# Performance work log

Hardware: AMD Instinct MI355X
Metric: run time of the kernel (lower is better)

The kernel has to match this reference:

```python
import jax, jax.numpy as jnp
import numpy as np

DIM = 2048
H = 16
DK = DIM // H   # head_k = 128
DV = DIM // H   # head_v = 128
B = 4
N = 4096
INV_SQRT_DK = 1.0 / float(np.sqrt(DK))


def setup_inputs() -> dict:
    key = jax.random.key(0)
    ks = jax.random.split(key, 12)
    s = 0.02
    return {
        "x": jax.random.normal(ks[0], (B, N, DIM), dtype=jnp.float32),
        "M_fast_prev": jax.random.normal(ks[1], (B, H, DK, DV), dtype=jnp.float32) * 0.05,
        "M_slow_prev": jax.random.normal(ks[2], (B, H, DK, DV), dtype=jnp.float32) * 0.05,
        "Wq": jax.random.normal(ks[3], (DIM, H * DK), dtype=jnp.float32) * s,
        "Wk": jax.random.normal(ks[4], (DIM, H * DK), dtype=jnp.float32) * s,
        "Wv": jax.random.normal(ks[5], (DIM, H * DV), dtype=jnp.float32) * s,
        "Wo": jax.random.normal(ks[6], (H * DV, DIM), dtype=jnp.float32) * s,
        "W_bilinear": jax.random.normal(ks[7], (H, DK, DK), dtype=jnp.float32) * 0.02,
        "fast_slope": jnp.full((H, 1, 1), 0.5, dtype=jnp.float32),
        "slow_slope": jnp.full((H, 1, 1), 0.01, dtype=jnp.float32),
        "inter_fast": jnp.full((H, 1, 1), 0.1, dtype=jnp.float32),
        "inter_slow": jnp.full((H, 1, 1), 0.9, dtype=jnp.float32),
        "S_fast": jax.random.normal(ks[8], (H, DK, DK), dtype=jnp.float32) * 0.05,
        "S_slow": jax.random.normal(ks[9], (H, DK, DK), dtype=jnp.float32) * 0.02,
        "f1_w": jax.random.normal(ks[10], (DIM, DIM // 2), dtype=jnp.float32) * s,
        "f1_b": jnp.zeros((DIM // 2,), dtype=jnp.float32),
        "f2_w": jax.random.normal(ks[11], (DIM // 2, H), dtype=jnp.float32) * s,
        "f2_b": jnp.zeros((H,), dtype=jnp.float32),
    }


def reference(x, M_fast_prev, M_slow_prev, Wq, Wk, Wv, Wo, W_bilinear,
              fast_slope, slow_slope, inter_fast, inter_slow,
              S_fast, S_slow, f1_w, f1_b, f2_w, f2_b):
    b, n, _ = x.shape
    # projections -> [b, h, n, d]
    q = (x @ Wq).reshape(b, n, H, DK).transpose(0, 2, 1, 3)
    k = (x @ Wk).reshape(b, n, H, DK).transpose(0, 2, 1, 3)
    v = (x @ Wv).reshape(b, n, H, DV).transpose(0, 2, 1, 3)

    # bilinear resonance modulation of keys
    resonance = jnp.tanh(jnp.einsum('bhnd,hde->bhne', k, W_bilinear))
    k_mod = k * (1.0 + 0.5 * resonance) * INV_SQRT_DK

    # exponential fast/slow decay weights over positions: [h, n, 1]
    idx = (jnp.arange(n, dtype=x.dtype) - (n - 1))[:, None]  # [n, 1]
    fast_w = jnp.exp(fast_slope * idx)  # [h, n, 1]
    slow_w = jnp.exp(slow_slope * idx)

    k_fast = k_mod * fast_w[None]  # [b, h, n, dk]
    k_slow = k_mod * slow_w[None]

    # outer-product state accumulation: [b, h, dk, dv]
    M_fast_curr = jnp.einsum('bhnd,bhnv->bhdv', k_fast, v)
    M_slow_curr = jnp.einsum('bhnd,bhnv->bhdv', k_slow, v)

    # inter-block state carry
    M_fast = M_fast_prev * inter_fast[None] + M_fast_curr
    M_slow = M_slow_prev * inter_slow[None] + M_slow_curr

    # refinement: (I + S) @ M
    eye = jnp.eye(DK, dtype=x.dtype)
    Mf_ref = jnp.einsum('hde,bhev->bhdv', eye[None] + S_fast, M_fast)
    Ms_ref = jnp.einsum('hde,bhev->bhdv', eye[None] + S_slow, M_slow)

    o_fast = jnp.einsum('bhnd,bhdv->bhnv', q, Mf_ref)
    o_slow = jnp.einsum('bhnd,bhdv->bhnv', q, Ms_ref)

    # flux gating from pooled tokens
    h1 = jax.nn.silu(x.mean(axis=1) @ f1_w + f1_b)
    psi = jax.nn.sigmoid(h1 @ f2_w + f2_b)  # [b, h]
    pe = psi[:, :, None, None]

    o_blend = (1.0 - pe) * o_fast + pe * o_slow  # [b, h, n, dv]
    o_blend = o_blend.transpose(0, 2, 1, 3).reshape(b, n, H * DV)
    out = o_blend @ Wo
    return out, M_fast, M_slow, psi
```

## Files before the change

### kernel.cpp

```cpp
#include <hip/hip_runtime.h>
#include <math.h>

typedef __bf16 bf16;
typedef __attribute__((ext_vector_type(8))) __bf16 bf16x8;
typedef __attribute__((ext_vector_type(4))) __bf16 bf16x4;
typedef __attribute__((ext_vector_type(2))) __bf16 bf16x2;
typedef __attribute__((ext_vector_type(4))) float f32x4;

#define DIM 2048
#define NH 16
#define DKK 128
#define BATCH 4
#define SEQ 4096
#define BN (BATCH*SEQ)
#define INV_SQRT_DK 0.08838834764831845f

#define MFMA16(a,b,c) __builtin_amdgcn_mfma_f32_16x16x32_bf16((a),(b),(c),0,0,0)

#define GLDS(gp, lp) __builtin_amdgcn_global_load_lds( \
    (const __attribute__((address_space(1))) void*)(gp), \
    (__attribute__((address_space(3))) void*)(lp), 16, 0, 0)

__device__ inline void stage_tile(const bf16* __restrict__ g, int ld,
                                  bf16* lds, int lane, int wave) {
  const int rl = lane >> 3;
  const int gc = ((lane & 7) ^ (rl & 7)) << 3;
  const bf16* gp = g + (size_t)(wave * 32 + rl) * ld + gc;
#pragma unroll
  for (int t = 0; t < 4; ++t)
    GLDS(gp + (size_t)(t * 8) * ld, lds + (wave * 32 + t * 8) * 64);
}

__device__ inline bf16x8 frag8(const bf16* lds, int r, int kc) {
  return *(const bf16x8*)(lds + r * 64 + (((kc ^ (r & 7)) << 3)));
}

__device__ inline bf16x8 frag8w(const bf16* lds, int r, int kc) {
  return *(const bf16x8*)(lds + r * 128 + (((kc ^ (r & 7)) << 3)));
}
__device__ inline int sqaddr(int r, int c) {
  return r * 128 + ((((c >> 3) ^ (r & 7)) << 3) | (c & 7));
}

__device__ inline float fast_exp(float x) { return __expf(x); }
__device__ inline float fast_tanh(float x) {
  float e2 = __expf(2.f * x);
  return 1.f - 2.f / (e2 + 1.f);
}

__global__ __launch_bounds__(256) void conv_bf16(const float* __restrict__ x,
                                                 bf16* __restrict__ y) {
  int i = (blockIdx.x * 256 + threadIdx.x) * 4;
  float4 v = *(const float4*)(x + i);
  bf16x4 o = { (bf16)v.x, (bf16)v.y, (bf16)v.z, (bf16)v.w };
  *(bf16x4*)(y + i) = o;
}

__global__ __launch_bounds__(256) void tconv3(const float* W0, const float* W1,
                                              const float* W2,
                                              bf16* O0, bf16* O1, bf16* O2) {
  __shared__ float tile[32][33];
  const float* Wp; bf16* Op;
  switch (blockIdx.z) {
    case 0: Wp = W0; Op = O0; break;
    case 1: Wp = W1; Op = O1; break;
    default: Wp = W2; Op = O2; break;
  }
  int c0 = blockIdx.x * 32, r0 = blockIdx.y * 32;
  int tx = threadIdx.x, ty = threadIdx.y;
#pragma unroll
  for (int i = 0; i < 4; ++i)
    tile[ty + i*8][tx] = Wp[(size_t)(r0 + ty + i*8) * DIM + c0 + tx];
  __syncthreads();
#pragma unroll
  for (int i = 0; i < 4; ++i)
    Op[(size_t)(c0 + ty + i*8) * DIM + r0 + tx] = (bf16)tile[tx][ty + i*8];
}

__global__ __launch_bounds__(256) void tconvWb(const float* __restrict__ W,
                                               bf16* __restrict__ Wt) {
  __shared__ float tile[32][33];
  const float* Wp = W + (size_t)blockIdx.z * DKK * DKK;
  bf16* Wtp = Wt + (size_t)blockIdx.z * DKK * DKK;
  int c0 = blockIdx.x * 32, r0 = blockIdx.y * 32;
  int tx = threadIdx.x, ty = threadIdx.y;
#pragma unroll
  for (int i = 0; i < 4; ++i)
    tile[ty + i*8][tx] = Wp[(size_t)(r0 + ty + i*8) * DKK + c0 + tx];
  __syncthreads();
#pragma unroll
  for (int i = 0; i < 4; ++i)
    Wtp[(size_t)(c0 + ty + i*8) * DKK + r0 + tx] = (bf16)tile[tx][ty + i*8];
}

__global__ __launch_bounds__(256) void rweights(const float* __restrict__ fs,
                                                const float* __restrict__ ss,
                                                float* __restrict__ rbuf) {
  int n = blockIdx.x * 256 + threadIdx.x;
  int h = blockIdx.y;
  rbuf[h * SEQ + n] = fast_exp((fs[h] - ss[h]) * (float)(n - (SEQ - 1)));
}

__global__ void zero_f32(float* p, int n) {
  int i = blockIdx.x * 256 + threadIdx.x;
  if (i < n) p[i] = 0.f;
}

__global__ __launch_bounds__(256) void mean_part(const bf16* __restrict__ xb,
                                                 float* __restrict__ xm) {
  int d0 = (blockIdx.x * 256 + threadIdx.x) * 2;
  int b = blockIdx.z;
  const bf16* xp = xb + ((size_t)b * SEQ + (size_t)blockIdx.y * 256) * DIM + d0;
  float s0 = 0.f, s1 = 0.f;
#pragma unroll 8
  for (int n = 0; n < 256; ++n) {
    bf16x2 v = *(const bf16x2*)(xp + (size_t)n * DIM);
    s0 += (float)v[0]; s1 += (float)v[1];
  }
  atomicAdd(&xm[b * DIM + d0], s0);
  atomicAdd(&xm[b * DIM + d0 + 1], s1);
}

__global__ __launch_bounds__(256) void mlp1(const float* __restrict__ xm,
                                            const float* __restrict__ f1w,
                                            float* __restrict__ h1raw) {
  int j = blockIdx.x * 256 + threadIdx.x;
  int b = blockIdx.y;
  int k0 = blockIdx.z * 256;
  const float* xmb = xm + b * DIM + k0;
  const float* w = f1w + (size_t)k0 * (DIM/2) + j;
  float s = 0.f;
#pragma unroll 4
  for (int k = 0; k < 256; ++k) s += xmb[k] * w[(size_t)k * (DIM/2)];
  atomicAdd(&h1raw[b * (DIM/2) + j], s);
}

__global__ void mlp2(const float* __restrict__ h1raw,
                     const float* __restrict__ f1b,
                     const float* __restrict__ f2w,
                     const float* __restrict__ f2b,
                     float* __restrict__ psi_out) {
  int t = threadIdx.x;
  int b = t >> 4, h = t & 15;
  float s = f2b[h];
  for (int k = 0; k < DIM/2; ++k) {
    float hv = h1raw[b * (DIM/2) + k] * (1.f / (float)SEQ) + f1b[k];
    hv = hv / (1.f + fast_exp(-hv));
    s += hv * f2w[k * NH + h];
  }
  psi_out[t] = 1.f / (1.f + fast_exp(-s));
}

template<int MODE>
__global__ __launch_bounds__(256) void gemm_bt(const bf16* __restrict__ A, int lda,
                                               const bf16* __restrict__ Bt, int ldb,
                                               void* __restrict__ Cv, int ldc, int K) {
  __shared__ bf16 sA[128 * 64];
  __shared__ bf16 sB[128 * 64];
  const int tid = threadIdx.x;
  const int lane = tid & 63;
  const int wave = tid >> 6;
  const int quad = lane >> 4;
  const int wm = (wave & 1) * 64;
  const int wn = (wave >> 1) * 64;
  const size_t m0 = (size_t)blockIdx.y * 128;
  const size_t n0 = (size_t)blockIdx.x * 128;
  const bf16* Ap = A;
  const bf16* Bp = Bt;
  size_t mrow = m0;
  size_t cbat = 0;
  if (MODE == 3) Bp += (size_t)(m0 >> 12) * DIM * DIM;
  if (MODE == 4) {
    size_t b = m0 >> 11;
    Ap += b * DIM * DIM;
    cbat = b * DIM * DIM;
    mrow = m0 & 2047;
  }
  f32x4 acc[4][4] = {};
  for (int k0 = 0; k0 < K; k0 += 64) {
    stage_tile(Ap + mrow * lda + k0, lda, sA, lane, wave);
    stage_tile(Bp + n0 * ldb + k0, ldb, sB, lane, wave);
    __syncthreads();
#pragma unroll
    for (int kk = 0; kk < 2; ++kk) {
      const int kc = kk * 4 + quad;
      bf16x8 af[4], bfr[4];
#pragma unroll
      for (int i = 0; i < 4; ++i) af[i] = frag8(sA, wm + i*16 + (lane & 15), kc);
#pragma unroll
      for (int j = 0; j < 4; ++j) bfr[j] = frag8(sB, wn + j*16 + (lane & 15), kc);
#pragma unroll
      for (int i = 0; i < 4; ++i)
#pragma unroll
        for (int j = 0; j < 4; ++j)
          acc[i][j] = MFMA16(af[i], bfr[j], acc[i][j]);
    }
    __syncthreads();
  }
  if (MODE == 2) {
    const int h = (int)(n0 >> 7) & (NH - 1);
    const int b = (int)(m0 >> 12);
    const int nbase0 = (int)(m0 & 4095) + wm + quad * 4;
    bf16* vt = (bf16*)Cv;
#pragma unroll
    for (int i = 0; i < 4; ++i)
#pragma unroll
      for (int j = 0; j < 4; ++j) {
        int dv = wn + j*16 + (lane & 15);
        bf16x4 p = { (bf16)acc[i][j][0], (bf16)acc[i][j][1],
                     (bf16)acc[i][j][2], (bf16)acc[i][j][3] };
        *(bf16x4*)(vt + ((size_t)(b * NH + h) * DKK + dv) * SEQ + nbase0 + i * 16) = p;
      }
  } else {
#pragma unroll
    for (int i = 0; i < 4; ++i)
#pragma unroll
      for (int j = 0; j < 4; ++j) {
        size_t col = n0 + wn + j*16 + (lane & 15);
        size_t row = mrow + wm + i*16 + quad * 4;
#pragma unroll
        for (int r = 0; r < 4; ++r) {
          if (MODE == 3) ((float*)Cv)[(row + r) * ldc + col] = acc[i][j][r];
          else           ((bf16*)Cv)[cbat + (row + r) * ldc + col] = (bf16)acc[i][j][r];
        }
      }
  }
}

__global__ __launch_bounds__(256) void gemm_k_res(const bf16* __restrict__ xb,
                                                  const bf16* __restrict__ Wtk,
                                                  const bf16* __restrict__ Wbt,
                                                  const float* __restrict__ slow_slope,
                                                  bf16* __restrict__ kts) {
  __shared__ bf16 smem[3 * 128 * 64];
  bf16* sA = smem;
  bf16* sB = smem + 8192;
  bf16* K2 = smem;
  bf16* sW = smem + 16384;
  const int tid = threadIdx.x;
  const int lane = tid & 63;
  const int wave = tid >> 6;
  const int quad = lane >> 4;
  const int wm = (wave & 1) * 64;
  const int wn = (wave >> 1) * 64;
  const int h = blockIdx.x;
  const size_t m0 = (size_t)blockIdx.y * 128;
  const int b = (int)(m0 >> 12);
  const int bh = b * NH + h;
  const float ss = slow_slope[h];

  const bf16* Ap = xb + m0 * DIM;
  const bf16* Bp = Wtk + (size_t)h * 128 * DIM;
  f32x4 acc[4][4] = {};
  for (int k0 = 0; k0 < DIM; k0 += 64) {
    stage_tile(Ap + k0, DIM, sA, lane, wave);
    stage_tile(Bp + k0, DIM, sB, lane, wave);
    __syncthreads();
#pragma unroll
    for (int kk = 0; kk < 2; ++kk) {
      const int kc = kk * 4 + quad;
      bf16x8 af[4], bfr[4];
#pragma unroll
      for (int i = 0; i < 4; ++i) af[i] = frag8(sA, wm + i*16 + (lane & 15), kc);
#pragma unroll
      for (int j = 0; j < 4; ++j) bfr[j] = frag8(sB, wn + j*16 + (lane & 15), kc);
#pragma unroll
      for (int i = 0; i < 4; ++i)
#pragma unroll
        for (int j = 0; j < 4; ++j)
          acc[i][j] = MFMA16(af[i], bfr[j], acc[i][j]);
    }
    __syncthreads();
  }
#pragma unroll
  for (int i = 0; i < 4; ++i)
#pragma unroll
    for (int j = 0; j < 4; ++j) {
      int c = wn + j*16 + (lane & 15);
#pragma unroll
      for (int r = 0; r < 4; ++r) {
        int row = wm + i*16 + quad*4 + r;
        K2[sqaddr(row, c)] = (bf16)acc[i][j][r];
      }
    }
  __syncthreads();
  f32x4 accR[4][4] = {};
  const bf16* Wp = Wbt + (size_t)h * DKK * DKK;
#pragma unroll
  for (int k0 = 0; k0 < 128; k0 += 64) {
    stage_tile(Wp + k0, DKK, sW, lane, wave);
    __syncthreads();
#pragma unroll
    for (int kk = 0; kk < 2; ++kk) {
      const int kcl = kk * 4 + quad;
      const int kcg = (k0 >> 3) + kcl;
      bf16x8 af[4], bfr[4];
#pragma unroll
      for (int i = 0; i < 4; ++i) af[i] = frag8w(K2, wm + i*16 + (lane & 15), kcg);
#pragma unroll
      for (int j = 0; j < 4; ++j) bfr[j] = frag8(sW, wn + j*16 + (lane & 15), kcl);
#pragma unroll
      for (int i = 0; i < 4; ++i)
#pragma unroll
        for (int j = 0; j < 4; ++j)
          accR[i][j] = MFMA16(af[i], bfr[j], accR[i][j]);
    }
    __syncthreads();
  }
  float wsv[4][4];
#pragma unroll
  for (int i = 0; i < 4; ++i)
#pragma unroll
    for (int r = 0; r < 4; ++r) {
      int nseq = (int)(m0 & 4095) + wm + i*16 + quad*4 + r;
      wsv[i][r] = fast_exp(ss * (float)(nseq - (SEQ - 1)));
    }
#pragma unroll
  for (int i = 0; i < 4; ++i)
#pragma unroll
    for (int j = 0; j < 4; ++j) {
      int c = wn + j*16 + (lane & 15);
      bf16x4 p;
#pragma unroll
      for (int r = 0; r < 4; ++r) {
        int row = wm + i*16 + quad*4 + r;
        float kv = (float)K2[sqaddr(row, c)];
        float res = fast_tanh(accR[i][j][r]);
        p[r] = (bf16)(kv * (1.f + 0.5f * res) * INV_SQRT_DK * wsv[i][r]);
      }
      int nbase = (int)(m0 & 4095) + wm + i*16 + quad*4;
      *(bf16x4*)(kts + ((size_t)bh * DKK + c) * SEQ + nbase) = p;
    }
}

__global__ __launch_bounds__(256) void mcurr(const bf16* __restrict__ kts,
                                             const bf16* __restrict__ vt,
                                             const float* __restrict__ rbuf,
                                             float* __restrict__ partials) {
  __shared__ bf16 sK[128 * 64];
  __shared__ bf16 sV[128 * 64];
  const int tid = threadIdx.x;
  const int lane = tid & 63;
  const int wave = tid >> 6;
  const int quad = lane >> 4;
  const int wm = (wave & 1) * 64, wn = (wave >> 1) * 64;
  const int s = blockIdx.x;
  const int bh = blockIdx.y;
  const int h = bh & (NH - 1);
  const bf16* Ap = kts + (size_t)bh * DKK * SEQ;
  const bf16* Bp = vt + (size_t)bh * DKK * SEQ;
  const float* rp = rbuf + (size_t)h * SEQ;
  f32x4 accF[4][4] = {}, accS[4][4] = {};
  for (int k0 = s * 512; k0 < s * 512 + 512; k0 += 64) {
    stage_tile(Ap + k0, SEQ, sK, lane, wave);
    stage_tile(Bp + k0, SEQ, sV, lane, wave);
    __syncthreads();
#pragma unroll
    for (int kk = 0; kk < 2; ++kk) {
      const int kc = kk * 4 + quad;
      const int kn = k0 + kc * 8;
      float rv[8];
      *(f32x4*)rv       = *(const f32x4*)(rp + kn);
      *(f32x4*)(rv + 4) = *(const f32x4*)(rp + kn + 4);
      bf16x8 afS[4], afF[4], bfv[4];
#pragma unroll
      for (int i = 0; i < 4; ++i) afS[i] = frag8(sK, wm + i*16 + (lane & 15), kc);
#pragma unroll
      for (int j = 0; j < 4; ++j) bfv[j] = frag8(sV, wn + j*16 + (lane & 15), kc);
#pragma unroll
      for (int i = 0; i < 4; ++i)
#pragma unroll
        for (int e = 0; e < 8; ++e)
          afF[i][e] = (bf16)((float)afS[i][e] * rv[e]);
#pragma unroll
      for (int i = 0; i < 4; ++i)
#pragma unroll
        for (int j = 0; j < 4; ++j) {
          accS[i][j] = MFMA16(afS[i], bfv[j], accS[i][j]);
          accF[i][j] = MFMA16(afF[i], bfv[j], accF[i][j]);
        }
    }
    __syncthreads();
  }
  float* Pf = partials + ((size_t)(s * 64 + bh) * 2 + 0) * (DKK * DKK);
  float* Ps = partials + ((size_t)(s * 64 + bh) * 2 + 1) * (DKK * DKK);
#pragma unroll
  for (int i = 0; i < 4; ++i)
#pragma unroll
    for (int j = 0; j < 4; ++j) {
      int col = wn + j*16 + (lane & 15);
      int row = wm + i*16 + quad * 4;
#pragma unroll
      for (int r = 0; r < 4; ++r) {
        Pf[(row + r) * DKK + col] = accF[i][j][r];
        Ps[(row + r) * DKK + col] = accS[i][j][r];
      }
    }
}

__global__ __launch_bounds__(256) void finalize(const float* __restrict__ partials,
                                                const float* __restrict__ Mf_prev,
                                                const float* __restrict__ Ms_prev,
                                                const float* __restrict__ inter_fast,
                                                const float* __restrict__ inter_slow,
                                                const float* __restrict__ S_fast,
                                                const float* __restrict__ S_slow,
                                                const float* __restrict__ psi,
                                                float* __restrict__ Mf_out,
                                                float* __restrict__ Ms_out,
                                                bf16* __restrict__ Mb) {
  __shared__ float sMf[128 * 33];
  __shared__ float sMs[128 * 33];
  const int t = threadIdx.x;
  const int bh = blockIdx.x;
  const int h = bh & (NH - 1);
  const int e0 = blockIdx.y * 32;
  const int el = t & 31;
  const int d0 = t >> 5;
  const float inf_ = inter_fast[h], ins_ = inter_slow[h];
  const size_t mb = (size_t)bh * (DKK * DKK);
#pragma unroll
  for (int i = 0; i < 16; ++i) {
    int d = d0 + 8 * i;
    int g = d * DKK + e0 + el;
    float mf = inf_ * Mf_prev[mb + g];
    float ms = ins_ * Ms_prev[mb + g];
#pragma unroll
    for (int s = 0; s < 8; ++s) {
      mf += partials[((size_t)(s * 64 + bh) * 2 + 0) * (DKK*DKK) + g];
      ms += partials[((size_t)(s * 64 + bh) * 2 + 1) * (DKK*DKK) + g];
    }
    Mf_out[mb + g] = mf;
    Ms_out[mb + g] = ms;
    sMf[d * 33 + el] = mf;
    sMs[d * 33 + el] = ms;
  }
  __syncthreads();
  const float p = psi[bh];
  for (int i = 0; i < 16; ++i) {
    int d = d0 + 8 * i;
    float accf = sMf[d * 33 + el];
    float accs = sMs[d * 33 + el];
    const float* Sf = S_fast + (size_t)h * (DKK*DKK) + (size_t)d * DKK;
    const float* Ss = S_slow + (size_t)h * (DKK*DKK) + (size_t)d * DKK;
    for (int k = 0; k < DKK; ++k) {
      accf += Sf[k] * sMf[k * 33 + el];
      accs += Ss[k] * sMs[k * 33 + el];
    }
    float blend = (1.f - p) * accf + p * accs;
    Mb[mb + (size_t)d * DKK + e0 + el] = (bf16)blend;
  }
}

__global__ __launch_bounds__(256) void w2_gemm(const bf16* __restrict__ Mb,
                                               const bf16* __restrict__ Wto,
                                               bf16* __restrict__ W2t) {
  __shared__ bf16 sA[128 * 64];
  __shared__ bf16 sB[128 * 64];
  const int tid = threadIdx.x;
  const int lane = tid & 63;
  const int wave = tid >> 6;
  const int quad = lane >> 4;
  const int wm = (wave & 1) * 64, wn = (wave >> 1) * 64;
  const int c0 = blockIdx.x * 128;
  const int bh = blockIdx.y;
  const int h = bh & (NH - 1), b = bh >> 4;
  const bf16* Ap = Mb + (size_t)bh * DKK * DKK;
  const bf16* Bp = Wto + (size_t)c0 * DIM + h * DKK;
  f32x4 acc[4][4] = {};
#pragma unroll
  for (int k0 = 0; k0 < DKK; k0 += 64) {
    stage_tile(Ap + k0, DKK, sA, lane, wave);
    stage_tile(Bp + k0, DIM, sB, lane, wave);
    __syncthreads();
#pragma unroll
    for (int kk = 0; kk < 2; ++kk) {
      const int kc = kk * 4 + quad;
      bf16x8 af[4], bfr[4];
#pragma unroll
      for (int i = 0; i < 4; ++i) af[i] = frag8(sA, wm + i*16 + (lane & 15), kc);
#pragma unroll
      for (int j = 0; j < 4; ++j) bfr[j] = frag8(sB, wn + j*16 + (lane & 15), kc);
#pragma unroll
      for (int i = 0; i < 4; ++i)
#pragma unroll
        for (int j = 0; j < 4; ++j)
          acc[i][j] = MFMA16(af[i], bfr[j], acc[i][j]);
    }
    __syncthreads();
  }
  bf16* base = W2t + (size_t)b * DIM * DIM + h * DKK;
#pragma unroll
  for (int i = 0; i < 4; ++i)
#pragma unroll
    for (int j = 0; j < 4; ++j) {
      int col = wn + j*16 + (lane & 15);
      int row0 = wm + i*16 + quad * 4;
      bf16x4 p = { (bf16)acc[i][j][0], (bf16)acc[i][j][1],
                   (bf16)acc[i][j][2], (bf16)acc[i][j][3] };
      *(bf16x4*)(base + (size_t)(c0 + col) * DIM + row0) = p;
    }
}

extern "C" void kernel_launch(void* const* d_in, const int* in_sizes, int n_in,
                              void* d_out, int out_size, void* d_ws, size_t ws_size,
                              hipStream_t stream) {
  const float* x        = (const float*)d_in[0];
  const float* Mf_prev  = (const float*)d_in[1];
  const float* Ms_prev  = (const float*)d_in[2];
  const float* Wq       = (const float*)d_in[3];
  const float* Wk       = (const float*)d_in[4];
  const float* Wv       = (const float*)d_in[5];
  const float* Wo       = (const float*)d_in[6];
  const float* Wbil     = (const float*)d_in[7];
  const float* fast_slope = (const float*)d_in[8];
  const float* slow_slope = (const float*)d_in[9];
  const float* inter_fast = (const float*)d_in[10];
  const float* inter_slow = (const float*)d_in[11];
  const float* S_fast   = (const float*)d_in[12];
  const float* S_slow   = (const float*)d_in[13];
  const float* f1w      = (const float*)d_in[14];
  const float* f1b      = (const float*)d_in[15];
  const float* f2w      = (const float*)d_in[16];
  const float* f2b      = (const float*)d_in[17];

  char* ws = (char*)d_ws;
  bf16*  xb       = (bf16*)(ws);
  float* partials = (float*)(ws + 67108864);
  bf16*  W2t      = (bf16*)(ws + 67108864);
  bf16*  Wcombt   = (bf16*)(ws + 100663296);
  bf16*  Wqb      = (bf16*)(ws + 134217728);
  bf16*  Wtk      = (bf16*)(ws + 142606336);
  bf16*  Wtv      = (bf16*)(ws + 150994944);
  bf16*  Wto      = (bf16*)(ws + 159383552);
  bf16*  Wbt      = (bf16*)(ws + 167772160);
  float* rbuf     = (float*)(ws + 168296448);
  bf16*  Mb       = (bf16*)(ws + 168558592);
  float* xm       = (float*)(ws + 170655744);
  float* h1raw    = (float*)(ws + 170688512);

  float* out  = (float*)d_out;
  float* MfO  = out + 33554432;
  float* MsO  = MfO + 1048576;
  float* psiO = MsO + 1048576;
  bf16* kts = (bf16*)d_out;
  bf16* vt  = kts + 33554432;

  conv_bf16<<<dim3(BN * DIM / 1024), 256, 0, stream>>>(x, xb);
  conv_bf16<<<dim3(DIM * DIM / 1024), 256, 0, stream>>>(Wq, Wqb);
  tconv3<<<dim3(64, 64, 3), dim3(32, 8), 0, stream>>>(Wk, Wv, Wo, Wtk, Wtv, Wto);
  tconvWb<<<dim3(4, 4, NH), dim3(32, 8), 0, stream>>>(Wbil, Wbt);
  rweights<<<dim3(16, 16), 256, 0, stream>>>(fast_slope, slow_slope, rbuf);

  zero_f32<<<dim3(48), 256, 0, stream>>>(xm, BATCH * DIM + BATCH * (DIM/2));
  mean_part<<<dim3(4, 16, 4), 256, 0, stream>>>(xb, xm);
  mlp1<<<dim3(4, 4, 8), 256, 0, stream>>>(xm, f1w, h1raw);
  mlp2<<<dim3(1), 64, 0, stream>>>(h1raw, f1b, f2w, f2b, psiO);

  gemm_bt<2><<<dim3(16, 128), 256, 0, stream>>>(xb, DIM, Wtv, DIM, vt, 0, DIM);
  gemm_k_res<<<dim3(16, 128), 256, 0, stream>>>(xb, Wtk, Wbt, slow_slope, kts);

  mcurr<<<dim3(8, 64), 256, 0, stream>>>(kts, vt, rbuf, partials);

  finalize<<<dim3(64, 4), 256, 0, stream>>>(partials, Mf_prev, Ms_prev, inter_fast,
                                            inter_slow, S_fast, S_slow, psiO,
                                            MfO, MsO, Mb);

  w2_gemm<<<dim3(16, 64), 256, 0, stream>>>(Mb, Wto, W2t);

  gemm_bt<4><<<dim3(16, 64), 256, 0, stream>>>(W2t, DIM, Wqb, DIM, Wcombt, DIM, DIM);

  gemm_bt<3><<<dim3(16, 128), 256, 0, stream>>>(xb, DIM, Wcombt, DIM, out, DIM, DIM);
}
```

Measured before the change: 1.232 ms.

## Use 256x256 double-buffered GEMM tiles and split K projection from resonance

Replaces the 128x128 single-buffered GEMM with a 256x256 tile kernel of 512 threads. It double-buffers LDS via global_load_lds, waits with partial vmcnt and raises MFMA priority with setprio. The fused K-projection-plus-resonance kernel is split: the K projection now uses the big GEMM writing bf16 into workspace, and a separate res_fuse kernel does the per-head bilinear tanh modulation. This raises data reuse and overlaps loads with compute, at the cost of an extra round trip of K through global memory and heavier register pressure (128 fp32 accumulators per thread).

```diff
diff --git a/kernel.cpp b/kernel.cpp
--- a/kernel.cpp
+++ b/kernel.cpp
@@ -35,11 +35,8 @@
   return *(const bf16x8*)(lds + r * 64 + (((kc ^ (r & 7)) << 3)));
 }
 
-__device__ inline bf16x8 frag8w(const bf16* lds, int r, int kc) {
-  return *(const bf16x8*)(lds + r * 128 + (((kc ^ (r & 7)) << 3)));
-}
-__device__ inline int sqaddr(int r, int c) {
-  return r * 128 + ((((c >> 3) ^ (r & 7)) << 3) | (c & 7));
+__device__ inline int sq64(int r, int c) {
+  return r * 64 + ((((c >> 3) ^ (r & 7)) << 3) | (c & 7));
 }
 
 __device__ inline float fast_exp(float x) { return __expf(x); }
@@ -152,19 +149,19 @@
 }
 
 template<int MODE>
-__global__ __launch_bounds__(256) void gemm_bt(const bf16* __restrict__ A, int lda,
-                                               const bf16* __restrict__ Bt, int ldb,
-                                               void* __restrict__ Cv, int ldc, int K) {
-  __shared__ bf16 sA[128 * 64];
-  __shared__ bf16 sB[128 * 64];
+__global__ __launch_bounds__(512, 2) void gemm256(const bf16* __restrict__ A, int lda,
+                                                  const bf16* __restrict__ Bt, int ldb,
+                                                  void* __restrict__ Cv, int ldc, int K) {
+  __shared__ bf16 smem[65536];
   const int tid = threadIdx.x;
   const int lane = tid & 63;
   const int wave = tid >> 6;
   const int quad = lane >> 4;
-  const int wm = (wave & 1) * 64;
-  const int wn = (wave >> 1) * 64;
-  const size_t m0 = (size_t)blockIdx.y * 128;
-  const size_t n0 = (size_t)blockIdx.x * 128;
+  const int l15 = lane & 15;
+  const int wm = (wave >> 2) * 128;
+  const int wn = (wave & 3) * 64;
+  const size_t m0 = (size_t)blockIdx.y * 256;
+  const size_t n0 = (size_t)blockIdx.x * 256;
   const bf16* Ap = A;
   const bf16* Bp = Bt;
   size_t mrow = m0;
@@ -172,52 +169,76 @@
   if (MODE == 3) Bp += (size_t)(m0 >> 12) * DIM * DIM;
   if (MODE == 4) {
     size_t b = m0 >> 11;
-    Ap += b * DIM * DIM;
-    cbat = b * DIM * DIM;
+    Ap += b * (size_t)DIM * DIM;
+    cbat = b * (size_t)DIM * DIM;
     mrow = m0 & 2047;
   }
-  f32x4 acc[4][4] = {};
-  for (int k0 = 0; k0 < K; k0 += 64) {
-    stage_tile(Ap + mrow * lda + k0, lda, sA, lane, wave);
-    stage_tile(Bp + n0 * ldb + k0, ldb, sB, lane, wave);
-    __syncthreads();
-#pragma unroll
-    for (int kk = 0; kk < 2; ++kk) {
-      const int kc = kk * 4 + quad;
-      bf16x8 af[4], bfr[4];
-#pragma unroll
-      for (int i = 0; i < 4; ++i) af[i] = frag8(sA, wm + i*16 + (lane & 15), kc);
-#pragma unroll
-      for (int j = 0; j < 4; ++j) bfr[j] = frag8(sB, wn + j*16 + (lane & 15), kc);
-#pragma unroll
-      for (int i = 0; i < 4; ++i)
-#pragma unroll
-        for (int j = 0; j < 4; ++j)
-          acc[i][j] = MFMA16(af[i], bfr[j], acc[i][j]);
-    }
-    __syncthreads();
+  const bf16* Arow = Ap + mrow * (size_t)lda;
+  const bf16* Brow = Bp + n0 * (size_t)ldb;
+  f32x4 acc[8][4] = {};
+  const int NT = K >> 6;
+  stage_tile(Arow, lda, smem, lane, wave);
+  stage_tile(Brow, ldb, smem + 32768, lane, wave);
+  for (int kt = 0; kt < NT; ++kt) {
+    const int cur = kt & 1;
+    const bf16* sA = smem + cur * 16384;
+    const bf16* sB = smem + 32768 + cur * 16384;
+    if (kt + 1 < NT) {
+      const int nxt = cur ^ 1;
+      const int k0 = (kt + 1) << 6;
+      stage_tile(Arow + k0, lda, smem + nxt * 16384, lane, wave);
+      stage_tile(Brow + k0, ldb, smem + 32768 + nxt * 16384, lane, wave);
+      asm volatile("s_waitcnt vmcnt(8)\n\ts_barrier" ::: "memory");
+    } else {
+      asm volatile("s_waitcnt vmcnt(0)\n\ts_barrier" ::: "memory");
+    }
+    bf16x8 bfr[2][4];
+#pragma unroll
+    for (int kk = 0; kk < 2; ++kk)
+#pragma unroll
+      for (int j = 0; j < 4; ++j)
+        bfr[kk][j] = frag8(sB, wn + j * 16 + l15, kk * 4 + quad);
+#pragma unroll
+    for (int i2 = 0; i2 < 4; ++i2) {
+      bf16x8 af[2][2];
+#pragma unroll
+      for (int ii = 0; ii < 2; ++ii)
+#pragma unroll
+        for (int kk = 0; kk < 2; ++kk)
+          af[ii][kk] = frag8(sA, wm + (i2 * 2 + ii) * 16 + l15, kk * 4 + quad);
+      __builtin_amdgcn_s_setprio(1);
+#pragma unroll
+      for (int ii = 0; ii < 2; ++ii)
+#pragma unroll
+        for (int j = 0; j < 4; ++j) {
+          acc[i2*2+ii][j] = MFMA16(af[ii][0], bfr[0][j], acc[i2*2+ii][j]);
+          acc[i2*2+ii][j] = MFMA16(af[ii][1], bfr[1][j], acc[i2*2+ii][j]);
+        }
+      __builtin_amdgcn_s_setprio(0);
+    }
+    asm volatile("s_barrier" ::: "memory");
   }
   if (MODE == 2) {
-    const int h = (int)(n0 >> 7) & (NH - 1);
-    const int b = (int)(m0 >> 12);
-    const int nbase0 = (int)(m0 & 4095) + wm + quad * 4;
+    const int bb = (int)(m0 >> 12);
+    const int nb0 = (int)(m0 & 4095) + wm + quad * 4;
     bf16* vt = (bf16*)Cv;
 #pragma unroll
-    for (int i = 0; i < 4; ++i)
+    for (int i = 0; i < 8; ++i)
 #pragma unroll
       for (int j = 0; j < 4; ++j) {
-        int dv = wn + j*16 + (lane & 15);
+        int colg = (int)n0 + wn + j * 16 + l15;
+        int h = colg >> 7, dv = colg & 127;
         bf16x4 p = { (bf16)acc[i][j][0], (bf16)acc[i][j][1],
                      (bf16)acc[i][j][2], (bf16)acc[i][j][3] };
-        *(bf16x4*)(vt + ((size_t)(b * NH + h) * DKK + dv) * SEQ + nbase0 + i * 16) = p;
+        *(bf16x4*)(vt + ((size_t)(bb * NH + h) * DKK + dv) * SEQ + nb0 + i * 16) = p;
       }
   } else {
 #pragma unroll
-    for (int i = 0; i < 4; ++i)
+    for (int i = 0; i < 8; ++i)
 #pragma unroll
       for (int j = 0; j < 4; ++j) {
-        size_t col = n0 + wn + j*16 + (lane & 15);
-        size_t row = mrow + wm + i*16 + quad * 4;
+        size_t col = n0 + wn + j * 16 + l15;
+        size_t row = mrow + wm + i * 16 + quad * 4;
 #pragma unroll
         for (int r = 0; r < 4; ++r) {
           if (MODE == 3) ((float*)Cv)[(row + r) * ldc + col] = acc[i][j][r];
@@ -227,43 +248,39 @@
   }
 }
 
-__global__ __launch_bounds__(256) void gemm_k_res(const bf16* __restrict__ xb,
-                                                  const bf16* __restrict__ Wtk,
-                                                  const bf16* __restrict__ Wbt,
-                                                  const float* __restrict__ slow_slope,
-                                                  bf16* __restrict__ kts) {
-  __shared__ bf16 smem[3 * 128 * 64];
-  bf16* sA = smem;
-  bf16* sB = smem + 8192;
-  bf16* K2 = smem;
-  bf16* sW = smem + 16384;
+__global__ __launch_bounds__(256) void res_fuse(const bf16* __restrict__ kn,
+                                                const bf16* __restrict__ Wbt,
+                                                const float* __restrict__ slow_slope,
+                                                bf16* __restrict__ kts) {
+  __shared__ bf16 sA2[2][8192];
+  __shared__ bf16 sB[8192];
   const int tid = threadIdx.x;
   const int lane = tid & 63;
   const int wave = tid >> 6;
   const int quad = lane >> 4;
+  const int l15 = lane & 15;
   const int wm = (wave & 1) * 64;
   const int wn = (wave >> 1) * 64;
-  const int h = blockIdx.x;
-  const size_t m0 = (size_t)blockIdx.y * 128;
-  const int b = (int)(m0 >> 12);
-  const int bh = b * NH + h;
+  const int nt = blockIdx.x;
+  const int bh = blockIdx.y;
+  const int h = bh & (NH - 1), b = bh >> 4;
+  const bf16* Ap = kn + ((size_t)b * SEQ + (size_t)nt * 128) * DIM + h * DKK;
+  const bf16* Bp = Wbt + (size_t)h * DKK * DKK;
   const float ss = slow_slope[h];
-
-  const bf16* Ap = xb + m0 * DIM;
-  const bf16* Bp = Wtk + (size_t)h * 128 * DIM;
   f32x4 acc[4][4] = {};
-  for (int k0 = 0; k0 < DIM; k0 += 64) {
-    stage_tile(Ap + k0, DIM, sA, lane, wave);
-    stage_tile(Bp + k0, DIM, sB, lane, wave);
+#pragma unroll
+  for (int c = 0; c < 2; ++c) {
+    stage_tile(Ap + c * 64, DIM, sA2[c], lane, wave);
+    stage_tile(Bp + c * 64, DKK, sB, lane, wave);
     __syncthreads();
 #pragma unroll
     for (int kk = 0; kk < 2; ++kk) {
       const int kc = kk * 4 + quad;
       bf16x8 af[4], bfr[4];
 #pragma unroll
-      for (int i = 0; i < 4; ++i) af[i] = frag8(sA, wm + i*16 + (lane & 15), kc);
-#pragma unroll
-      for (int j = 0; j < 4; ++j) bfr[j] = frag8(sB, wn + j*16 + (lane & 15), kc);
+      for (int i = 0; i < 4; ++i) af[i] = frag8(sA2[c], wm + i*16 + l15, kc);
+#pragma unroll
+      for (int j = 0; j < 4; ++j) bfr[j] = frag8(sB, wn + j*16 + l15, kc);
 #pragma unroll
       for (int i = 0; i < 4; ++i)
 #pragma unroll
@@ -272,64 +289,30 @@
     }
     __syncthreads();
   }
+  float wsv[4][4];
+#pragma unroll
+  for (int i = 0; i < 4; ++i)
+#pragma unroll
+    for (int r = 0; r < 4; ++r) {
+      int ng = nt * 128 + wm + i*16 + quad*4 + r;
+      wsv[i][r] = fast_exp(ss * (float)(ng - (SEQ - 1)));
+    }
 #pragma unroll
   for (int i = 0; i < 4; ++i)
 #pragma unroll
     for (int j = 0; j < 4; ++j) {
-      int c = wn + j*16 + (lane & 15);
+      int e = wn + j*16 + l15;
+      const bf16* sAe = sA2[e >> 6];
+      int ec = e & 63;
+      bf16x4 p;
 #pragma unroll
       for (int r = 0; r < 4; ++r) {
-        int row = wm + i*16 + quad*4 + r;
-        K2[sqaddr(row, c)] = (bf16)acc[i][j][r];
-      }
-    }
-  __syncthreads();
-  f32x4 accR[4][4] = {};
-  const bf16* Wp = Wbt + (size_t)h * DKK * DKK;
-#pragma unroll
-  for (int k0 = 0; k0 < 128; k0 += 64) {
-    stage_tile(Wp + k0, DKK, sW, lane, wave);
-    __syncthreads();
-#pragma unroll
-    for (int kk = 0; kk < 2; ++kk) {
-      const int kcl = kk * 4 + quad;
-      const int kcg = (k0 >> 3) + kcl;
-      bf16x8 af[4], bfr[4];
-#pragma unroll
-      for (int i = 0; i < 4; ++i) af[i] = frag8w(K2, wm + i*16 + (lane & 15), kcg);
-#pragma unroll
-      for (int j = 0; j < 4; ++j) bfr[j] = frag8(sW, wn + j*16 + (lane & 15), kcl);
-#pragma unroll
-      for (int i = 0; i < 4; ++i)
-#pragma unroll
-        for (int j = 0; j < 4; ++j)
-          accR[i][j] = MFMA16(af[i], bfr[j], accR[i][j]);
-    }
-    __syncthreads();
-  }
-  float wsv[4][4];
-#pragma unroll
-  for (int i = 0; i < 4; ++i)
-#pragma unroll
-    for (int r = 0; r < 4; ++r) {
-      int nseq = (int)(m0 & 4095) + wm + i*16 + quad*4 + r;
-      wsv[i][r] = fast_exp(ss * (float)(nseq - (SEQ - 1)));
-    }
-#pragma unroll
-  for (int i = 0; i < 4; ++i)
-#pragma unroll
-    for (int j = 0; j < 4; ++j) {
-      int c = wn + j*16 + (lane & 15);
-      bf16x4 p;
-#pragma unroll
-      for (int r = 0; r < 4; ++r) {
-        int row = wm + i*16 + quad*4 + r;
-        float kv = (float)K2[sqaddr(row, c)];
-        float res = fast_tanh(accR[i][j][r]);
+        int nl = wm + i*16 + quad*4 + r;
+        float kv = (float)sAe[sq64(nl, ec)];
+        float res = fast_tanh(acc[i][j][r]);
         p[r] = (bf16)(kv * (1.f + 0.5f * res) * INV_SQRT_DK * wsv[i][r]);
       }
-      int nbase = (int)(m0 & 4095) + wm + i*16 + quad*4;
-      *(bf16x4*)(kts + ((size_t)bh * DKK + c) * SEQ + nbase) = p;
+      *(bf16x4*)(kts + ((size_t)bh * DKK + e) * SEQ + nt * 128 + wm + i*16 + quad*4) = p;
     }
 }
 
@@ -358,10 +341,10 @@
 #pragma unroll
     for (int kk = 0; kk < 2; ++kk) {
       const int kc = kk * 4 + quad;
-      const int kn = k0 + kc * 8;
+      const int kn_ = k0 + kc * 8;
       float rv[8];
-      *(f32x4*)rv       = *(const f32x4*)(rp + kn);
-      *(f32x4*)(rv + 4) = *(const f32x4*)(rp + kn + 4);
+      *(f32x4*)rv       = *(const f32x4*)(rp + kn_);
+      *(f32x4*)(rv + 4) = *(const f32x4*)(rp + kn_ + 4);
       bf16x8 afS[4], afF[4], bfv[4];
 #pragma unroll
       for (int i = 0; i < 4; ++i) afS[i] = frag8(sK, wm + i*16 + (lane & 15), kc);
@@ -526,6 +509,7 @@
 
   char* ws = (char*)d_ws;
   bf16*  xb       = (bf16*)(ws);
+  bf16*  kn       = (bf16*)(ws + 67108864);
   float* partials = (float*)(ws + 67108864);
   bf16*  W2t      = (bf16*)(ws + 67108864);
   bf16*  Wcombt   = (bf16*)(ws + 100663296);
@@ -557,8 +541,10 @@
   mlp1<<<dim3(4, 4, 8), 256, 0, stream>>>(xm, f1w, h1raw);
   mlp2<<<dim3(1), 64, 0, stream>>>(h1raw, f1b, f2w, f2b, psiO);
 
-  gemm_bt<2><<<dim3(16, 128), 256, 0, stream>>>(xb, DIM, Wtv, DIM, vt, 0, DIM);
-  gemm_k_res<<<dim3(16, 128), 256, 0, stream>>>(xb, Wtk, Wbt, slow_slope, kts);
+  gemm256<2><<<dim3(8, 64), 512, 0, stream>>>(xb, DIM, Wtv, DIM, vt, 0, DIM);
+  gemm256<5><<<dim3(8, 64), 512, 0, stream>>>(xb, DIM, Wtk, DIM, kn, DIM, DIM);
+
+  res_fuse<<<dim3(32, 64), 256, 0, stream>>>(kn, Wbt, slow_slope, kts);
 
   mcurr<<<dim3(8, 64), 256, 0, stream>>>(kts, vt, rbuf, partials);
 
@@ -568,7 +554,7 @@
 
   w2_gemm<<<dim3(16, 64), 256, 0, stream>>>(Mb, Wto, W2t);
 
-  gemm_bt<4><<<dim3(16, 64), 256, 0, stream>>>(W2t, DIM, Wqb, DIM, Wcombt, DIM, DIM);
-
-  gemm_bt<3><<<dim3(16, 128), 256, 0, stream>>>(xb, DIM, Wcombt, DIM, out, DIM, DIM);
-}
+  gemm256<4><<<dim3(8, 32), 512, 0, stream>>>(W2t, DIM, Wqb, DIM, Wcombt, DIM, DIM);
+
+  gemm256<3><<<dim3(8, 64), 512, 0, stream>>>(xb, DIM, Wcombt, DIM, out, DIM, DIM);
+}
```

New measurement: 1.138 ms. 7.7% less time.
